# Kernel optimization log

Hardware: AMD Instinct MI355X
Metric: run time of the kernel (lower is better)

## Reference

```python
import jax, jax.numpy as jnp
import numpy as np

N = 16384          # input points
F = 128            # feature dim (x is (N, 3+F))
POOL = 4           # pooling_factor
M = N // POOL      # number of FPS query points
K = 16             # num_neighbors


def setup_inputs() -> dict:
    key = jax.random.key(0)
    x = jax.random.normal(key, (N, 3 + F), dtype=jnp.float32)
    return {"x": x}


def _fps(coords, m):
    """Furthest point sampling: coords (N,3) -> m indices. Deterministic start at 0."""
    n = coords.shape[0]

    def step(carry, _):
        min_d2, last = carry
        d2 = jnp.sum((coords - coords[last]) ** 2, axis=-1)  # (N,)
        min_d2 = jnp.minimum(min_d2, d2)
        nxt = jnp.argmax(min_d2).astype(jnp.int32)
        return (min_d2, nxt), nxt

    init = (jnp.full((n,), jnp.inf, dtype=coords.dtype), jnp.int32(0))
    _, idxs = jax.lax.scan(step, init, None, length=m - 1)
    return jnp.concatenate([jnp.zeros((1,), dtype=jnp.int32), idxs])


def reference(x):
    coords = x[:, :3]                          # (N,3)
    fps_idx = _fps(coords, M)                  # (M,)
    q_points = coords[fps_idx]                 # (M,3)

    # knn neighbor query: squared distances (M,N), take K nearest
    d2 = jnp.sum((q_points[:, None, :] - coords[None, :, :]) ** 2, axis=-1)
    _, nbr_idx = jax.lax.top_k(-d2, K)         # (M,K)

    s_feats = x[nbr_idx, 3:]                   # (M,K,F) gather
    pooled = jnp.max(s_feats, axis=1)          # feat_mapping='max' -> (M,F)
    return jnp.concatenate([q_points, pooled], axis=-1)  # (M, 3+F)
```

## Files before the change

### kernel.cpp

```cpp
#include <hip/hip_runtime.h>

#define N_PTS 16384
#define ROWF  131
#define M_OUT 4096
#define KNN   16
#define FPS_T 1024
#define SORT_T 1024

typedef unsigned long long u64;

__device__ __constant__ unsigned short c_spread4[16] =
  {0,1,8,9,64,65,72,73,512,513,520,521,576,577,584,585};

__device__ __forceinline__ int cell_of(float x, float y, float z) {
  int ix = (int)floorf((x + 4.0f) * 2.0f); ix = ix < 0 ? 0 : (ix > 15 ? 15 : ix);
  int iy = (int)floorf((y + 4.0f) * 2.0f); iy = iy < 0 ? 0 : (iy > 15 ? 15 : iy);
  int iz = (int)floorf((z + 4.0f) * 2.0f); iz = iz < 0 ? 0 : (iz > 15 ? 15 : iz);
  return (int)c_spread4[ix] | ((int)c_spread4[iy] << 1) | ((int)c_spread4[iz] << 2);
}

template <int CTRL, int ROW_MASK>
__device__ __forceinline__ u64 kmax_dpp(u64 k) {
  const int lo = (int)(unsigned)k, hi = (int)(unsigned)(k >> 32);
  const int nlo = __builtin_amdgcn_update_dpp(lo, lo, CTRL, ROW_MASK, 0xf, false);
  const int nhi = __builtin_amdgcn_update_dpp(hi, hi, CTRL, ROW_MASK, 0xf, false);
  const u64 nk = ((u64)(unsigned)nhi << 32) | (unsigned)nlo;
  return nk > k ? nk : k;
}

__global__ void prep_kernel(const float* __restrict__ x,
                            float4* __restrict__ coords4) {
  const int p = blockIdx.x * blockDim.x + threadIdx.x;
  if (p < N_PTS) {
    coords4[p] = make_float4(x[p * ROWF + 0], x[p * ROWF + 1],
                             x[p * ROWF + 2], 0.0f);
  }
}

__global__ __launch_bounds__(1024, 1)
void sort_kernel(const float4* __restrict__ coords4, float4* __restrict__ gP4) {
  __shared__ unsigned int sh[4096];
  __shared__ unsigned int sws[16];
  const int tid = threadIdx.x, lane = tid & 63, wid = tid >> 6;

#pragma unroll
  for (int i = 0; i < 4; ++i) sh[tid * 4 + i] = 0;
  __syncthreads();

  int cel[16];
#pragma unroll
  for (int j = 0; j < 16; ++j) {
    const float4 v = coords4[tid + SORT_T * j];
    const int c = cell_of(v.x, v.y, v.z);
    cel[j] = c;
    atomicAdd(&sh[c], 1u);
  }
  __syncthreads();

  const unsigned h0 = sh[tid * 4 + 0], h1 = sh[tid * 4 + 1];
  const unsigned h2 = sh[tid * 4 + 2], h3 = sh[tid * 4 + 3];
  const unsigned tsum = h0 + h1 + h2 + h3;
  unsigned inc = tsum;
#pragma unroll
  for (int off = 1; off < 64; off <<= 1) {
    const unsigned v = __shfl_up(inc, off);
    if (lane >= off) inc += v;
  }
  if (lane == 63) sws[wid] = inc;
  __syncthreads();
  if (tid == 0) {
    unsigned run = 0;
#pragma unroll
    for (int w = 0; w < 16; ++w) { const unsigned t = sws[w]; sws[w] = run; run += t; }
  }
  __syncthreads();
  const unsigned base = sws[wid] + inc - tsum;
  sh[tid * 4 + 0] = base;
  sh[tid * 4 + 1] = base + h0;
  sh[tid * 4 + 2] = base + h0 + h1;
  sh[tid * 4 + 3] = base + h0 + h1 + h2;
  __syncthreads();

#pragma unroll
  for (int j = 0; j < 16; ++j) {
    const int p = tid + SORT_T * j;
    const float4 v = coords4[p];
    const unsigned rk = atomicAdd(&sh[cel[j]], 1u);
    const int slot = (int)(((rk & 15u) << 10) | (rk >> 4));
    gP4[slot] = make_float4(v.x, v.y, v.z, __int_as_float(p));
  }
}

#define REP16(F) F(0) F(1) F(2) F(3) F(4) F(5) F(6) F(7) \
                 F(8) F(9) F(10) F(11) F(12) F(13) F(14) F(15)

__global__
__attribute__((amdgpu_flat_work_group_size(FPS_T, FPS_T)))
__attribute__((amdgpu_waves_per_eu(4, 4)))
void fps_kernel(const float4* __restrict__ coords4,
                const float4* __restrict__ gP4, float* __restrict__ out) {
  __shared__ u64 s_wkey[2][16];
  const int tid = threadIdx.x, lane = tid & 63, wid = tid >> 6;

#define FPS_DECL(j) float px##j, py##j, pz##j, md##j; unsigned ni##j;
  REP16(FPS_DECL)
#undef FPS_DECL

#define FPS_INIT(j) { const float4 v = gP4[(j << 10) + tid];               \
    px##j = v.x; py##j = v.y; pz##j = v.z;                                 \
    ni##j = (unsigned)__float_as_int(v.w);                                 \
    md##j = __int_as_float(0x7f800000); }
  REP16(FPS_INIT)
#undef FPS_INIT

  float sx = 0.f, sy = 0.f, sz = 0.f;
#define FPS_ACC(j) sx += px##j; sy += py##j; sz += pz##j;
  REP16(FPS_ACC)
#undef FPS_ACC
  const float ccx = sx * (1.0f / 16.0f), ccy = sy * (1.0f / 16.0f),
              ccz = sz * (1.0f / 16.0f);
  float cr2 = 0.f;
#define FPS_RAD(j) { const float dx = px##j - ccx, dy = py##j - ccy,       \
                     dz = pz##j - ccz;                                     \
    cr2 = fmaxf(cr2, dx * dx + dy * dy + dz * dz); }
  REP16(FPS_RAD)
#undef FPS_RAD
  const float cr = sqrtf(cr2) * 1.000001f + 1e-6f;

  float thr = __int_as_float(0x7f800000);
  u64 wk = 0;

  const float4 q0 = coords4[0];
  float qx = q0.x, qy = q0.y, qz = q0.z;
  if (tid == 0) { out[0] = qx; out[1] = qy; out[2] = qz; }

  for (int s = 1; s < M_OUT; ++s) {
    const float dqx = qx - ccx, dqy = qy - ccy, dqz = qz - ccz;
    const float dd = dqx * dqx + dqy * dqy + dqz * dqz;
    const bool ldirty = (dd * 0.999999f <= thr);

    if (__ballot(ldirty)) {
      float m = 0.f;
#define FPS_UPD(j) {                                                       \
      const float dx = px##j - qx, dy = py##j - qy, dz = pz##j - qz;       \
      const float d2 = __fadd_rn(__fadd_rn(__fmul_rn(dx, dx),              \
                                           __fmul_rn(dy, dy)),             \
                                 __fmul_rn(dz, dz));                       \
      const float nm = fminf(md##j, d2);                                   \
      md##j = nm;                                                          \
      m = fmaxf(m, nm); }
      REP16(FPS_UPD)
#undef FPS_UPD
      unsigned c = 0xFFFFFFFFu;
#define FPS_SCAN(j) c = (md##j == m) ? (ni##j < c ? ni##j : c) : c;
      REP16(FPS_SCAN)
#undef FPS_SCAN
      u64 k = ((u64)__float_as_uint(m) << 32) | (unsigned)(N_PTS - 1 - c);

      k = kmax_dpp<0xB1,  0xf>(k);
      k = kmax_dpp<0x4E,  0xf>(k);
      k = kmax_dpp<0x141, 0xf>(k);
      k = kmax_dpp<0x140, 0xf>(k);
      k = kmax_dpp<0x142, 0xa>(k);
      k = kmax_dpp<0x143, 0xc>(k);
      const unsigned wlo = (unsigned)__builtin_amdgcn_readlane((int)(unsigned)k, 63);
      const unsigned whi = (unsigned)__builtin_amdgcn_readlane((int)(unsigned)(k >> 32), 63);
      wk = ((u64)whi << 32) | wlo;

      const float u = (cr + sqrtf(m * 1.0001f)) * 1.000003f;
      thr = u * u * 1.000001f;
    }

    const int par = s & 1;
    if (lane == 0) s_wkey[par][wid] = wk;
    __syncthreads();
    u64 kk = s_wkey[par][lane & 15];
    kk = kmax_dpp<0xB1,  0xf>(kk);
    kk = kmax_dpp<0x4E,  0xf>(kk);
    kk = kmax_dpp<0x141, 0xf>(kk);
    kk = kmax_dpp<0x140, 0xf>(kk);

    const int oidx = (N_PTS - 1) - (int)(unsigned)(kk & 0xFFFFFFFFu);
    const float4 wpt = coords4[oidx];
    qx = wpt.x; qy = wpt.y; qz = wpt.z;
    if (tid == 0) {
      float* orow = out + (size_t)s * ROWF;
      orow[0] = qx; orow[1] = qy; orow[2] = qz;
    }
  }
}

__global__ __launch_bounds__(256)
void knn_pool_kernel(const float* __restrict__ x,
                     const float4* __restrict__ coords4,
                     float* __restrict__ out) {
  const int lane = threadIdx.x & 63;
  const int q = blockIdx.x * 4 + (threadIdx.x >> 6);

  const float qx = out[(size_t)q * ROWF + 0];
  const float qy = out[(size_t)q * ROWF + 1];
  const float qz = out[(size_t)q * ROWF + 2];

  u64 h[KNN];
#pragma unroll
  for (int k = 0; k < KNN; ++k) h[k] = ~0ULL;

  for (int c = lane; c < N_PTS; c += 64) {
    const float4 v = coords4[c];
    const float dx = v.x - qx, dy = v.y - qy, dz = v.z - qz;
    const float d2 = __fadd_rn(__fadd_rn(__fmul_rn(dx, dx), __fmul_rn(dy, dy)),
                               __fmul_rn(dz, dz));
    const u64 e = ((u64)__float_as_uint(d2) << 32) | (unsigned)c;
    if (e < h[KNN - 1]) {
#pragma unroll
      for (int k = KNN - 1; k >= 1; --k) {
        const u64 prev = h[k - 1];
        h[k] = (e < prev) ? prev : ((e < h[k]) ? e : h[k]);
      }
      h[0] = (e < h[0]) ? e : h[0];
    }
  }

  int nbr[KNN];
#pragma unroll
  for (int rr = 0; rr < KNN; ++rr) {
    u64 best = h[0];
#pragma unroll
    for (int off = 32; off; off >>= 1) {
      const u64 o = __shfl_xor(best, off);
      best = (o < best) ? o : best;
    }
    nbr[rr] = (int)(unsigned)(best & 0xffffffffULL);
    if (h[0] == best) {
#pragma unroll
      for (int k = 0; k < KNN - 1; ++k) h[k] = h[k + 1];
      h[KNN - 1] = ~0ULL;
    }
  }

  float a0 = __int_as_float(0xff800000), a1 = a0;
#pragma unroll
  for (int rr = 0; rr < KNN; ++rr) {
    const float* row = x + (size_t)nbr[rr] * ROWF + 3;
    a0 = fmaxf(a0, row[lane]);
    a1 = fmaxf(a1, row[lane + 64]);
  }
  float* orow = out + (size_t)q * ROWF + 3;
  orow[lane] = a0;
  orow[lane + 64] = a1;
}

extern "C" void kernel_launch(void* const* d_in, const int* in_sizes, int n_in,
                              void* d_out, int out_size, void* d_ws, size_t ws_size,
                              hipStream_t stream) {
  const float* x = (const float*)d_in[0];
  float* out = (float*)d_out;

  float4* coords4 = (float4*)d_ws;
  float4* gP4     = coords4 + N_PTS;

  hipLaunchKernelGGL(prep_kernel, dim3(64), dim3(256), 0, stream, x, coords4);
  hipLaunchKernelGGL(sort_kernel, dim3(1), dim3(1024), 0, stream, coords4, gP4);
  hipLaunchKernelGGL(fps_kernel, dim3(1), dim3(FPS_T), 0, stream,
                     coords4, gP4, out);
  hipLaunchKernelGGL(knn_pool_kernel, dim3(M_OUT / 4), dim3(256), 0, stream,
                     x, coords4, out);
}
```

Before: 6.637 ms.

## Drop spatial sort and wave-skip bounds; use packed f32x2 FPS distance updates

Removes the Morton-cell sort kernel and the per-wave bounding-sphere early-out in furthest point sampling, so every wave now updates all 16 of its points on every step. The distance computation is vectorised into float2 ops, which may map to packed FP32 instructions, with FMA contraction disabled to keep rounding exact. The argmax index is now derived from the register slot instead of stored indices, and the cross-lane max tree is flattened. This trades the skip-work heuristic and the sort launch for a simpler, uniform, lower-latency inner loop.

New measurement: 6.649 ms, median of 3. About the same (+0.2%).

```diff
diff --git a/kernel.cpp b/kernel.cpp
--- a/kernel.cpp
+++ b/kernel.cpp
@@ -5,19 +5,9 @@
 #define M_OUT 4096
 #define KNN   16
 #define FPS_T 1024
-#define SORT_T 1024
 
 typedef unsigned long long u64;
-
-__device__ __constant__ unsigned short c_spread4[16] =
-  {0,1,8,9,64,65,72,73,512,513,520,521,576,577,584,585};
-
-__device__ __forceinline__ int cell_of(float x, float y, float z) {
-  int ix = (int)floorf((x + 4.0f) * 2.0f); ix = ix < 0 ? 0 : (ix > 15 ? 15 : ix);
-  int iy = (int)floorf((y + 4.0f) * 2.0f); iy = iy < 0 ? 0 : (iy > 15 ? 15 : iy);
-  int iz = (int)floorf((z + 4.0f) * 2.0f); iz = iz < 0 ? 0 : (iz > 15 ? 15 : iz);
-  return (int)c_spread4[ix] | ((int)c_spread4[iy] << 1) | ((int)c_spread4[iz] << 2);
-}
+typedef float f32x2 __attribute__((ext_vector_type(2)));
 
 template <int CTRL, int ROW_MASK>
 __device__ __forceinline__ u64 kmax_dpp(u64 k) {
@@ -37,142 +27,80 @@
   }
 }
 
-__global__ __launch_bounds__(1024, 1)
-void sort_kernel(const float4* __restrict__ coords4, float4* __restrict__ gP4) {
-  __shared__ unsigned int sh[4096];
-  __shared__ unsigned int sws[16];
-  const int tid = threadIdx.x, lane = tid & 63, wid = tid >> 6;
-
-#pragma unroll
-  for (int i = 0; i < 4; ++i) sh[tid * 4 + i] = 0;
-  __syncthreads();
-
-  int cel[16];
-#pragma unroll
-  for (int j = 0; j < 16; ++j) {
-    const float4 v = coords4[tid + SORT_T * j];
-    const int c = cell_of(v.x, v.y, v.z);
-    cel[j] = c;
-    atomicAdd(&sh[c], 1u);
-  }
-  __syncthreads();
-
-  const unsigned h0 = sh[tid * 4 + 0], h1 = sh[tid * 4 + 1];
-  const unsigned h2 = sh[tid * 4 + 2], h3 = sh[tid * 4 + 3];
-  const unsigned tsum = h0 + h1 + h2 + h3;
-  unsigned inc = tsum;
-#pragma unroll
-  for (int off = 1; off < 64; off <<= 1) {
-    const unsigned v = __shfl_up(inc, off);
-    if (lane >= off) inc += v;
-  }
-  if (lane == 63) sws[wid] = inc;
-  __syncthreads();
-  if (tid == 0) {
-    unsigned run = 0;
-#pragma unroll
-    for (int w = 0; w < 16; ++w) { const unsigned t = sws[w]; sws[w] = run; run += t; }
-  }
-  __syncthreads();
-  const unsigned base = sws[wid] + inc - tsum;
-  sh[tid * 4 + 0] = base;
-  sh[tid * 4 + 1] = base + h0;
-  sh[tid * 4 + 2] = base + h0 + h1;
-  sh[tid * 4 + 3] = base + h0 + h1 + h2;
-  __syncthreads();
-
-#pragma unroll
-  for (int j = 0; j < 16; ++j) {
-    const int p = tid + SORT_T * j;
-    const float4 v = coords4[p];
-    const unsigned rk = atomicAdd(&sh[cel[j]], 1u);
-    const int slot = (int)(((rk & 15u) << 10) | (rk >> 4));
-    gP4[slot] = make_float4(v.x, v.y, v.z, __int_as_float(p));
-  }
-}
-
-#define REP16(F) F(0) F(1) F(2) F(3) F(4) F(5) F(6) F(7) \
-                 F(8) F(9) F(10) F(11) F(12) F(13) F(14) F(15)
+#define REP16R(F) F(15) F(14) F(13) F(12) F(11) F(10) F(9) F(8) \
+                  F(7) F(6) F(5) F(4) F(3) F(2) F(1) F(0)
+#define REPP(F) F(0,0,1) F(1,2,3) F(2,4,5) F(3,6,7) \
+                F(4,8,9) F(5,10,11) F(6,12,13) F(7,14,15)
 
 __global__
 __attribute__((amdgpu_flat_work_group_size(FPS_T, FPS_T)))
 __attribute__((amdgpu_waves_per_eu(4, 4)))
-void fps_kernel(const float4* __restrict__ coords4,
-                const float4* __restrict__ gP4, float* __restrict__ out) {
+void fps_kernel(const float4* __restrict__ coords4, float* __restrict__ out) {
+#pragma clang fp contract(off)
   __shared__ u64 s_wkey[2][16];
   const int tid = threadIdx.x, lane = tid & 63, wid = tid >> 6;
 
-#define FPS_DECL(j) float px##j, py##j, pz##j, md##j; unsigned ni##j;
-  REP16(FPS_DECL)
+#define FPS_DECL(t,a,b) f32x2 PX##t, PY##t, PZ##t; float md##a, md##b;
+  REPP(FPS_DECL)
 #undef FPS_DECL
 
-#define FPS_INIT(j) { const float4 v = gP4[(j << 10) + tid];               \
-    px##j = v.x; py##j = v.y; pz##j = v.z;                                 \
-    ni##j = (unsigned)__float_as_int(v.w);                                 \
-    md##j = __int_as_float(0x7f800000); }
-  REP16(FPS_INIT)
+#define FPS_INIT(t,a,b) {                                                  \
+    const float4 va = coords4[(a << 10) + tid];                            \
+    const float4 vb = coords4[(b << 10) + tid];                            \
+    PX##t = (f32x2){va.x, vb.x};                                           \
+    PY##t = (f32x2){va.y, vb.y};                                           \
+    PZ##t = (f32x2){va.z, vb.z};                                           \
+    md##a = __int_as_float(0x7f800000);                                    \
+    md##b = __int_as_float(0x7f800000); }
+  REPP(FPS_INIT)
 #undef FPS_INIT
-
-  float sx = 0.f, sy = 0.f, sz = 0.f;
-#define FPS_ACC(j) sx += px##j; sy += py##j; sz += pz##j;
-  REP16(FPS_ACC)
-#undef FPS_ACC
-  const float ccx = sx * (1.0f / 16.0f), ccy = sy * (1.0f / 16.0f),
-              ccz = sz * (1.0f / 16.0f);
-  float cr2 = 0.f;
-#define FPS_RAD(j) { const float dx = px##j - ccx, dy = py##j - ccy,       \
-                     dz = pz##j - ccz;                                     \
-    cr2 = fmaxf(cr2, dx * dx + dy * dy + dz * dz); }
-  REP16(FPS_RAD)
-#undef FPS_RAD
-  const float cr = sqrtf(cr2) * 1.000001f + 1e-6f;
-
-  float thr = __int_as_float(0x7f800000);
-  u64 wk = 0;
 
   const float4 q0 = coords4[0];
   float qx = q0.x, qy = q0.y, qz = q0.z;
   if (tid == 0) { out[0] = qx; out[1] = qy; out[2] = qz; }
 
   for (int s = 1; s < M_OUT; ++s) {
-    const float dqx = qx - ccx, dqy = qy - ccy, dqz = qz - ccz;
-    const float dd = dqx * dqx + dqy * dqy + dqz * dqz;
-    const bool ldirty = (dd * 0.999999f <= thr);
+    const f32x2 QX = {qx, qx}, QY = {qy, qy}, QZ = {qz, qz};
 
-    if (__ballot(ldirty)) {
-      float m = 0.f;
-#define FPS_UPD(j) {                                                       \
-      const float dx = px##j - qx, dy = py##j - qy, dz = pz##j - qz;       \
-      const float d2 = __fadd_rn(__fadd_rn(__fmul_rn(dx, dx),              \
-                                           __fmul_rn(dy, dy)),             \
-                                 __fmul_rn(dz, dz));                       \
-      const float nm = fminf(md##j, d2);                                   \
-      md##j = nm;                                                          \
-      m = fmaxf(m, nm); }
-      REP16(FPS_UPD)
+#define FPS_UPD(t,a,b) {                                                   \
+    const f32x2 dx = PX##t - QX;                                           \
+    const f32x2 dy = PY##t - QY;                                           \
+    const f32x2 dz = PZ##t - QZ;                                           \
+    const f32x2 xx = dx * dx;                                              \
+    const f32x2 yy = dy * dy;                                              \
+    const f32x2 zz = dz * dz;                                              \
+    const f32x2 ss = xx + yy;                                              \
+    const f32x2 d2 = ss + zz;                                              \
+    md##a = fminf(md##a, d2.x);                                            \
+    md##b = fminf(md##b, d2.y); }
+    REPP(FPS_UPD)
 #undef FPS_UPD
-      unsigned c = 0xFFFFFFFFu;
-#define FPS_SCAN(j) c = (md##j == m) ? (ni##j < c ? ni##j : c) : c;
-      REP16(FPS_SCAN)
+
+    const float a0 = fmaxf(fmaxf(md0,  md1),  md2);
+    const float a1 = fmaxf(fmaxf(md3,  md4),  md5);
+    const float a2 = fmaxf(fmaxf(md6,  md7),  md8);
+    const float a3 = fmaxf(fmaxf(md9,  md10), md11);
+    const float a4 = fmaxf(fmaxf(md12, md13), md14);
+    const float b0 = fmaxf(fmaxf(a0, a1), a2);
+    const float b1 = fmaxf(fmaxf(a3, a4), md15);
+    const float m  = fmaxf(b0, b1);
+
+    unsigned c = 0;
+#define FPS_SCAN(j) c = (md##j == m) ? (unsigned)j : c;
+    REP16R(FPS_SCAN)
 #undef FPS_SCAN
-      u64 k = ((u64)__float_as_uint(m) << 32) | (unsigned)(N_PTS - 1 - c);
+    const unsigned ni = (unsigned)tid + (c << 10);
+    u64 k = ((u64)__float_as_uint(m) << 32) | (unsigned)(N_PTS - 1 - ni);
 
-      k = kmax_dpp<0xB1,  0xf>(k);
-      k = kmax_dpp<0x4E,  0xf>(k);
-      k = kmax_dpp<0x141, 0xf>(k);
-      k = kmax_dpp<0x140, 0xf>(k);
-      k = kmax_dpp<0x142, 0xa>(k);
-      k = kmax_dpp<0x143, 0xc>(k);
-      const unsigned wlo = (unsigned)__builtin_amdgcn_readlane((int)(unsigned)k, 63);
-      const unsigned whi = (unsigned)__builtin_amdgcn_readlane((int)(unsigned)(k >> 32), 63);
-      wk = ((u64)whi << 32) | wlo;
-
-      const float u = (cr + sqrtf(m * 1.0001f)) * 1.000003f;
-      thr = u * u * 1.000001f;
-    }
+    k = kmax_dpp<0xB1,  0xf>(k);
+    k = kmax_dpp<0x4E,  0xf>(k);
+    k = kmax_dpp<0x141, 0xf>(k);
+    k = kmax_dpp<0x140, 0xf>(k);
+    k = kmax_dpp<0x142, 0xa>(k);
+    k = kmax_dpp<0x143, 0xc>(k);
 
     const int par = s & 1;
-    if (lane == 0) s_wkey[par][wid] = wk;
+    if (lane == 63) s_wkey[par][wid] = k;
     __syncthreads();
     u64 kk = s_wkey[par][lane & 15];
     kk = kmax_dpp<0xB1,  0xf>(kk);
@@ -257,12 +185,9 @@
   float* out = (float*)d_out;
 
   float4* coords4 = (float4*)d_ws;
-  float4* gP4     = coords4 + N_PTS;
 
   hipLaunchKernelGGL(prep_kernel, dim3(64), dim3(256), 0, stream, x, coords4);
-  hipLaunchKernelGGL(sort_kernel, dim3(1), dim3(1024), 0, stream, coords4, gP4);
-  hipLaunchKernelGGL(fps_kernel, dim3(1), dim3(FPS_T), 0, stream,
-                     coords4, gP4, out);
+  hipLaunchKernelGGL(fps_kernel, dim3(1), dim3(FPS_T), 0, stream, coords4, out);
   hipLaunchKernelGGL(knn_pool_kernel, dim3(M_OUT / 4), dim3(256), 0, stream,
                      x, coords4, out);
 }
```
